# Kernel optimization log

Measured on AMD Instinct MI355X. Metric: run time of the kernel, lower is better.

The kernel has to match this reference:

```python
import jax, jax.numpy as jnp
import numpy as np

N_QUBITS = 4
N_LAYERS = 3
DIM = 2 ** N_QUBITS  # 16 amplitudes; qubit 0 is the most-significant bit
BATCH = 262144

# bit of qubit q in basis index: (idx >> (N_QUBITS-1-q)) & 1
_bits = (np.arange(DIM)[:, None] >> np.arange(N_QUBITS - 1, -1, -1)[None, :]) & 1  # [16,4]

# circular CZ entangler diagonal: CZ(0,1),CZ(1,2),CZ(2,3),CZ(0,3)
_sign = np.ones(DIM)
for p, q in [(0, 1), (1, 2), (2, 3), (0, 3)]:
    _sign *= 1.0 - 2.0 * (_bits[:, p] * _bits[:, q])
CZ_DIAG = jnp.asarray(_sign, jnp.complex64)           # [16]
ZMAT = jnp.asarray(1 - 2 * _bits, jnp.float32)        # [16,4], <Z_q> signs


def _rx(t):
    c = jnp.cos(t / 2).astype(jnp.complex64)
    js = (-1j) * jnp.sin(t / 2).astype(jnp.complex64)
    return jnp.stack([jnp.stack([c, js], -1), jnp.stack([js, c], -1)], -2)


def _ry(t):
    c = jnp.cos(t / 2).astype(jnp.complex64)
    s = jnp.sin(t / 2).astype(jnp.complex64)
    return jnp.stack([jnp.stack([c, -s], -1), jnp.stack([s, c], -1)], -2)


def _rz(t):
    ph = jnp.exp(-0.5j * t.astype(jnp.complex64))
    z = jnp.zeros_like(ph)
    return jnp.stack([jnp.stack([ph, z], -1), jnp.stack([z, jnp.conj(ph)], -1)], -2)


def _apply(psi, M, q):
    # psi: [B, 16] complex64, M: [2,2] (shared) or [B,2,2] (per-sample)
    L, R = 2 ** q, 2 ** (N_QUBITS - 1 - q)
    B = psi.shape[0]
    psi = psi.reshape(B, L, 2, R)
    eq = 'ij,bljr->blir' if M.ndim == 2 else 'bij,bljr->blir'
    return jnp.einsum(eq, M, psi).reshape(B, DIM)


def setup_inputs() -> dict:
    key = jax.random.key(0)
    k1, k2 = jax.random.split(key)
    x = jax.random.normal(k1, (BATCH, N_QUBITS), dtype=jnp.float32)
    theta = jax.random.uniform(k2, (1, 3 * (N_LAYERS + 1) * N_QUBITS),
                               minval=0.0, maxval=np.pi, dtype=jnp.float32)
    lmbd = jnp.ones((N_QUBITS * N_LAYERS,), dtype=jnp.float32)
    return {"x": x, "theta": theta, "lmbd": lmbd}


def reference(x, theta, lmbd):
    B = x.shape[0]
    params = theta.reshape(N_LAYERS + 1, N_QUBITS, 3)
    # tiled inputs scaled by trainable lambdas: a[b,l,i] = lmbd[l*4+i] * x[b,i]
    a = lmbd.reshape(N_LAYERS, N_QUBITS)[None] * x[:, None, :]  # [B,3,4]
    # activation = 'linear' -> identity
    psi = jnp.zeros((B, DIM), jnp.complex64).at[:, 0].set(1.0)
    for l in range(N_LAYERS):
        # variational single-qubit rotations (shared across batch)
        for i in range(N_QUBITS):
            psi = _apply(psi, _rx(params[l, i, 0]), i)
            psi = _apply(psi, _ry(params[l, i, 1]), i)
            psi = _apply(psi, _rz(params[l, i, 2]), i)
        # circular CZ entangler (diagonal)
        psi = psi * CZ_DIAG
        # data re-uploading (per-sample angles)
        for i in range(N_QUBITS):
            psi = _apply(psi, _rx(a[:, l, i]), i)
        for i in range(N_QUBITS):
            psi = _apply(psi, _ry(a[:, l, i]), i)
        zang = (a[:, l, 0], a[:, l, 0], a[:, l, 1], a[:, l, 1])
        for i in range(N_QUBITS):
            psi = _apply(psi, _rz(zang[i]), i)
        # trailing variational rotations with last-layer params (applied every layer)
        for i in range(N_QUBITS):
            psi = _apply(psi, _rx(params[N_LAYERS, i, 0]), i)
            psi = _apply(psi, _ry(params[N_LAYERS, i, 1]), i)
            psi = _apply(psi, _rz(params[N_LAYERS, i, 2]), i)
    probs = psi.real ** 2 + psi.imag ** 2  # [B,16]
    return probs @ ZMAT                    # [B,4] <Z_q> expectations
```

## Files before the change

kernel.cpp:

```cpp
#include <hip/hip_runtime.h>

#define BATCH 262144
#define BLOCK 256

struct c2f { float re, im; };

__device__ __forceinline__ c2f cmul(c2f a, c2f b){
    return { a.re*b.re - a.im*b.im, a.re*b.im + a.im*b.re };
}
__device__ __forceinline__ c2f cmulc(c2f a, c2f b){
    return { a.re*b.re + a.im*b.im, a.im*b.re - a.re*b.im };
}
__device__ __forceinline__ void su2mul(c2f a1, c2f b1, c2f a2, c2f b2, c2f& ao, c2f& bo){
    c2f t1 = cmul(a1, a2), t2 = cmulc(b1, b2);
    ao = { t1.re - t2.re, t1.im - t2.im };
    c2f t3 = cmul(a1, b2), t4 = cmulc(b1, a2);
    bo = { t3.re + t4.re, t3.im + t4.im };
}
__device__ __forceinline__ int czneg(int s){
    int b0 = (s >> 3) & 1, b1 = (s >> 2) & 1, b2 = (s >> 1) & 1, b3 = s & 1;
    return (b0 & b1) ^ (b1 & b2) ^ (b2 & b3) ^ (b0 & b3);
}

__global__ __launch_bounds__(BLOCK) void vqc_kernel(
    const float* __restrict__ x,
    const float* __restrict__ theta,
    const float* __restrict__ lmbd,
    float* __restrict__ out)
{
    __shared__ float2 sU[4][4][2];
    __shared__ float2 sA[3][4][2];
    __shared__ float2 sPsi0[16];
    __shared__ float  sL[12];

    const int tid = threadIdx.x;

    if (tid < 16) {
        int l = tid >> 2, q = tid & 3;
        float t0 = 0.5f * theta[(l * 4 + q) * 3 + 0];
        float t1 = 0.5f * theta[(l * 4 + q) * 3 + 1];
        float t2 = 0.5f * theta[(l * 4 + q) * 3 + 2];
        float c0, s0, c1, s1, c2v, s2v;
        __sincosf(t0, &s0, &c0);
        __sincosf(t1, &s1, &c1);
        __sincosf(t2, &s2v, &c2v);
        c2f aP = { c1 * c0, s1 * s0 };
        c2f bP = { -s1 * c0, -c1 * s0 };
        c2f ph = { c2v, -s2v };
        c2f aU = cmul(ph, aP);
        c2f bU = cmul(ph, bP);
        sU[l][q][0] = make_float2(aU.re, aU.im);
        sU[l][q][1] = make_float2(bU.re, bU.im);
    }
    if (tid < 12) sL[tid] = lmbd[tid];
    __syncthreads();

    if (tid < 12) {
        int k = tid >> 2, q = tid & 3;
        c2f aW = { sU[3][q][0].x, sU[3][q][0].y };
        c2f bW = { sU[3][q][1].x, sU[3][q][1].y };
        c2f aA = aW, bA = bW;
        if (k < 2) {
            c2f aN = { sU[k + 1][q][0].x, sU[k + 1][q][0].y };
            c2f bN = { sU[k + 1][q][1].x, sU[k + 1][q][1].y };
            su2mul(aN, bN, aW, bW, aA, bA);
        }
        sA[k][q][0] = make_float2(aA.re, aA.im);
        sA[k][q][1] = make_float2(bA.re, bA.im);
    }
    if (tid >= 16 && tid < 32) {
        int s = tid - 16;
        c2f v = { 1.f, 0.f };
        #pragma unroll
        for (int q = 0; q < 4; ++q) {
            int bit = (s >> (3 - q)) & 1;
            c2f a = { sU[0][q][0].x, sU[0][q][0].y };
            c2f b = { sU[0][q][1].x, sU[0][q][1].y };
            c2f e = bit ? c2f{ -b.re, b.im } : a;
            v = cmul(v, e);
        }
        if (czneg(s)) { v.re = -v.re; v.im = -v.im; }
        sPsi0[s] = make_float2(v.re, v.im);
    }
    __syncthreads();

    const int b = blockIdx.x * BLOCK + tid;
    float4 xr = ((const float4*)x)[b];
    float xv[4] = { xr.x, xr.y, xr.z, xr.w };

    float prr[16], pii[16];
    #pragma unroll
    for (int s = 0; s < 16; ++s) { float2 v = sPsi0[s]; prr[s] = v.x; pii[s] = v.y; }

    #pragma unroll
    for (int k = 0; k < 3; ++k) {
        float ch[4], sh[4];
        #pragma unroll
        for (int q = 0; q < 4; ++q) {
            float h = 0.5f * sL[k * 4 + q] * xv[q];
            __sincosf(h, &sh[q], &ch[q]);
        }
        #pragma unroll
        for (int q = 0; q < 4; ++q) {
            float c = ch[q], s = sh[q];
            int zq = q >> 1;
            float cz = ch[zq], sz = sh[zq];
            float cc = c * c, ss = s * s, cs = c * s;
            c2f aV = { cc * cz + ss * sz, ss * cz - cc * sz };
            c2f bV = { -cs * (cz + sz), -cs * (cz - sz) };
            float2 fa = sA[k][q][0], fb = sA[k][q][1];
            c2f aA = { fa.x, fa.y }, bA = { fb.x, fb.y };
            c2f aM, bM;
            su2mul(aA, bA, aV, bV, aM, bM);
            const int R = 8 >> q;
            #pragma unroll
            for (int g = 0; g < 8; ++g) {
                int low = g & (R - 1);
                int s0i = ((g - low) << 1) | low;
                int s1i = s0i + R;
                float p0r = prr[s0i], p0i = pii[s0i];
                float p1r = prr[s1i], p1i = pii[s1i];
                prr[s0i] =  aM.re * p0r - aM.im * p0i + bM.re * p1r - bM.im * p1i;
                pii[s0i] =  aM.re * p0i + aM.im * p0r + bM.re * p1i + bM.im * p1r;
                prr[s1i] = -bM.re * p0r - bM.im * p0i + aM.re * p1r + aM.im * p1i;
                pii[s1i] = -bM.re * p0i + bM.im * p0r + aM.re * p1i - aM.im * p1r;
            }
        }
        if (k < 2) {
            #pragma unroll
            for (int s = 0; s < 16; ++s) {
                if (czneg(s)) { prr[s] = -prr[s]; pii[s] = -pii[s]; }
            }
        }
    }

    float o0 = 0.f, o1 = 0.f, o2 = 0.f, o3 = 0.f;
    #pragma unroll
    for (int s = 0; s < 16; ++s) {
        float p = prr[s] * prr[s] + pii[s] * pii[s];
        o0 += ((s >> 3) & 1) ? -p : p;
        o1 += ((s >> 2) & 1) ? -p : p;
        o2 += ((s >> 1) & 1) ? -p : p;
        o3 += ((s >> 0) & 1) ? -p : p;
    }
    float4 ov;
    ov.x = o0; ov.y = o1; ov.z = o2; ov.w = o3;
    ((float4*)out)[b] = ov;
}

extern "C" void kernel_launch(void* const* d_in, const int* in_sizes, int n_in,
                              void* d_out, int out_size, void* d_ws, size_t ws_size,
                              hipStream_t stream) {
    const float* x     = (const float*)d_in[0];
    const float* theta = (const float*)d_in[1];
    const float* lmbd  = (const float*)d_in[2];
    float* out = (float*)d_out;
    vqc_kernel<<<dim3(BATCH / BLOCK), dim3(BLOCK), 0, stream>>>(x, theta, lmbd, out);
}
```

Baseline: 79.80 us.

## Process two samples per thread with packed float2 math and hardware sin/cos

Each thread now handles two batch samples (t and t+HALF) stored as paired floats, so the compiler can emit packed FP32 ops (v_pk_fma/v_pk_mul) on CDNA. Sin/cos use the native amdgcn sin/cos builtins with the angle pre-scaled to revolutions, and the final Z-expectation reduction is rewritten as a butterfly of sums and differences. The grid is halved. This aims to cut the ALU instruction count per sample, at the cost of higher register pressure (64 state floats per thread) and fewer threads in flight.

```diff
diff --git a/kernel.cpp b/kernel.cpp
--- a/kernel.cpp
+++ b/kernel.cpp
@@ -1,10 +1,10 @@
 #include <hip/hip_runtime.h>
 
 #define BATCH 262144
+#define HALF  (BATCH / 2)
 #define BLOCK 256
 
 struct c2f { float re, im; };
-
 __device__ __forceinline__ c2f cmul(c2f a, c2f b){
     return { a.re*b.re - a.im*b.im, a.re*b.im + a.im*b.re };
 }
@@ -22,6 +22,29 @@
     return (b0 & b1) ^ (b1 & b2) ^ (b2 & b3) ^ (b0 & b3);
 }
 
+struct p2 { float x, y; };
+__device__ __forceinline__ p2 operator+(p2 a, p2 b){ return { a.x + b.x, a.y + b.y }; }
+__device__ __forceinline__ p2 operator-(p2 a, p2 b){ return { a.x - b.x, a.y - b.y }; }
+__device__ __forceinline__ p2 operator*(p2 a, p2 b){ return { a.x * b.x, a.y * b.y }; }
+__device__ __forceinline__ p2 operator-(p2 a){ return { -a.x, -a.y }; }
+__device__ __forceinline__ p2 splat(float f){ return { f, f }; }
+
+struct cp { p2 re, im; };
+__device__ __forceinline__ cp cpmul(cp a, cp b){
+    return { a.re*b.re - a.im*b.im, a.re*b.im + a.im*b.re };
+}
+__device__ __forceinline__ cp cpmulc(cp a, cp b){
+    return { a.re*b.re + a.im*b.im, a.im*b.re - a.re*b.im };
+}
+__device__ __forceinline__ void su2mulp(cp a1, cp b1, cp a2, cp b2, cp& ao, cp& bo){
+    cp t1 = cpmul(a1, a2), t2 = cpmulc(b1, b2);
+    ao = { t1.re - t2.re, t1.im - t2.im };
+    cp t3 = cpmul(a1, b2), t4 = cpmulc(b1, a2);
+    bo = { t3.re + t4.re, t3.im + t4.im };
+}
+
+#define INV2PI 0.15915494309189535f
+
 __global__ __launch_bounds__(BLOCK) void vqc_kernel(
     const float* __restrict__ x,
     const float* __restrict__ theta,
@@ -31,7 +54,7 @@
     __shared__ float2 sU[4][4][2];
     __shared__ float2 sA[3][4][2];
     __shared__ float2 sPsi0[16];
-    __shared__ float  sL[12];
+    __shared__ float  sRev[12];
 
     const int tid = threadIdx.x;
 
@@ -52,7 +75,7 @@
         sU[l][q][0] = make_float2(aU.re, aU.im);
         sU[l][q][1] = make_float2(bU.re, bU.im);
     }
-    if (tid < 12) sL[tid] = lmbd[tid];
+    if (tid < 12) sRev[tid] = (0.5f * INV2PI) * lmbd[tid];
     __syncthreads();
 
     if (tid < 12) {
@@ -84,46 +107,53 @@
     }
     __syncthreads();
 
-    const int b = blockIdx.x * BLOCK + tid;
-    float4 xr = ((const float4*)x)[b];
-    float xv[4] = { xr.x, xr.y, xr.z, xr.w };
+    const int t = blockIdx.x * BLOCK + tid;
+    float4 xa = ((const float4*)x)[t];
+    float4 xb = ((const float4*)x)[t + HALF];
+    p2 xv[4] = { {xa.x, xb.x}, {xa.y, xb.y}, {xa.z, xb.z}, {xa.w, xb.w} };
 
-    float prr[16], pii[16];
+    p2 prr[16], pii[16];
     #pragma unroll
-    for (int s = 0; s < 16; ++s) { float2 v = sPsi0[s]; prr[s] = v.x; pii[s] = v.y; }
+    for (int s = 0; s < 16; ++s) {
+        float2 v = sPsi0[s];
+        prr[s] = splat(v.x);
+        pii[s] = splat(v.y);
+    }
 
     #pragma unroll
     for (int k = 0; k < 3; ++k) {
-        float ch[4], sh[4];
+        p2 ch[4], sh[4];
         #pragma unroll
         for (int q = 0; q < 4; ++q) {
-            float h = 0.5f * sL[k * 4 + q] * xv[q];
-            __sincosf(h, &sh[q], &ch[q]);
+            p2 rev = xv[q] * splat(sRev[k * 4 + q]);
+            sh[q] = { __builtin_amdgcn_sinf(rev.x), __builtin_amdgcn_sinf(rev.y) };
+            ch[q] = { __builtin_amdgcn_cosf(rev.x), __builtin_amdgcn_cosf(rev.y) };
         }
         #pragma unroll
         for (int q = 0; q < 4; ++q) {
-            float c = ch[q], s = sh[q];
-            int zq = q >> 1;
-            float cz = ch[zq], sz = sh[zq];
-            float cc = c * c, ss = s * s, cs = c * s;
-            c2f aV = { cc * cz + ss * sz, ss * cz - cc * sz };
-            c2f bV = { -cs * (cz + sz), -cs * (cz - sz) };
+            p2 c = ch[q], s = sh[q];
+            const int zq = q >> 1;
+            p2 cz = ch[zq], sz = sh[zq];
+            p2 cc = c * c, ss = s * s, cs = c * s;
+            cp aV = { cc * cz + ss * sz, ss * cz - cc * sz };
+            cp bV = { -(cs * (cz + sz)), -(cs * (cz - sz)) };
             float2 fa = sA[k][q][0], fb = sA[k][q][1];
-            c2f aA = { fa.x, fa.y }, bA = { fb.x, fb.y };
-            c2f aM, bM;
-            su2mul(aA, bA, aV, bV, aM, bM);
+            cp aA = { splat(fa.x), splat(fa.y) };
+            cp bA = { splat(fb.x), splat(fb.y) };
+            cp aM, bM;
+            su2mulp(aA, bA, aV, bV, aM, bM);
             const int R = 8 >> q;
             #pragma unroll
             for (int g = 0; g < 8; ++g) {
                 int low = g & (R - 1);
                 int s0i = ((g - low) << 1) | low;
                 int s1i = s0i + R;
-                float p0r = prr[s0i], p0i = pii[s0i];
-                float p1r = prr[s1i], p1i = pii[s1i];
-                prr[s0i] =  aM.re * p0r - aM.im * p0i + bM.re * p1r - bM.im * p1i;
-                pii[s0i] =  aM.re * p0i + aM.im * p0r + bM.re * p1i + bM.im * p1r;
-                prr[s1i] = -bM.re * p0r - bM.im * p0i + aM.re * p1r + aM.im * p1i;
-                pii[s1i] = -bM.re * p0i + bM.im * p0r + aM.re * p1i - aM.im * p1r;
+                p2 p0r = prr[s0i], p0i = pii[s0i];
+                p2 p1r = prr[s1i], p1i = pii[s1i];
+                prr[s0i] = aM.re * p0r - aM.im * p0i + bM.re * p1r - bM.im * p1i;
+                pii[s0i] = aM.re * p0i + aM.im * p0r + bM.re * p1i + bM.im * p1r;
+                prr[s1i] = aM.re * p1r + aM.im * p1i - bM.re * p0r - bM.im * p0i;
+                pii[s1i] = aM.re * p1i - aM.im * p1r - bM.re * p0i + bM.im * p0r;
             }
         }
         if (k < 2) {
@@ -134,18 +164,25 @@
         }
     }
 
-    float o0 = 0.f, o1 = 0.f, o2 = 0.f, o3 = 0.f;
+    p2 p[16];
     #pragma unroll
-    for (int s = 0; s < 16; ++s) {
-        float p = prr[s] * prr[s] + pii[s] * pii[s];
-        o0 += ((s >> 3) & 1) ? -p : p;
-        o1 += ((s >> 2) & 1) ? -p : p;
-        o2 += ((s >> 1) & 1) ? -p : p;
-        o3 += ((s >> 0) & 1) ? -p : p;
-    }
-    float4 ov;
-    ov.x = o0; ov.y = o1; ov.z = o2; ov.w = o3;
-    ((float4*)out)[b] = ov;
+    for (int s = 0; s < 16; ++s) p[s] = prr[s] * prr[s] + pii[s] * pii[s];
+
+    p2 s01[8], d01[8];
+    #pragma unroll
+    for (int i = 0; i < 8; ++i) { s01[i] = p[2*i] + p[2*i+1]; d01[i] = p[2*i] - p[2*i+1]; }
+    p2 o3 = ((d01[0] + d01[1]) + (d01[2] + d01[3])) + ((d01[4] + d01[5]) + (d01[6] + d01[7]));
+    p2 s2v[4], d2v[4];
+    #pragma unroll
+    for (int j = 0; j < 4; ++j) { s2v[j] = s01[2*j] + s01[2*j+1]; d2v[j] = s01[2*j] - s01[2*j+1]; }
+    p2 o2 = (d2v[0] + d2v[1]) + (d2v[2] + d2v[3]);
+    p2 o1 = (s2v[0] - s2v[1]) + (s2v[2] - s2v[3]);
+    p2 o0 = (s2v[0] + s2v[1]) - (s2v[2] + s2v[3]);
+
+    float4 oa = { o0.x, o1.x, o2.x, o3.x };
+    float4 ob = { o0.y, o1.y, o2.y, o3.y };
+    ((float4*)out)[t] = oa;
+    ((float4*)out)[t + HALF] = ob;
 }
 
 extern "C" void kernel_launch(void* const* d_in, const int* in_sizes, int n_in,
@@ -155,5 +192,5 @@
     const float* theta = (const float*)d_in[1];
     const float* lmbd  = (const float*)d_in[2];
     float* out = (float*)d_out;
-    vqc_kernel<<<dim3(BATCH / BLOCK), dim3(BLOCK), 0, stream>>>(x, theta, lmbd, out);
+    vqc_kernel<<<dim3(HALF / BLOCK), dim3(BLOCK), 0, stream>>>(x, theta, lmbd, out);
 }
```

Measured after the change: 81.55 us. 2.2% more time.
